# Kernel tuning notes

Measured on AMD Instinct MI355X. Metric: run time of the kernel, lower is better.

The kernel has to match this reference:

```python
import jax, jax.numpy as jnp
import numpy as np
from jax import lax

K = 3  # kernel_size


def _dynamic_conv(x, kernel, k, d):
    """Involution-style dynamic depthwise conv.
    x: [N,C,H,W], kernel: [N,C,k*k,H,W] per-pixel weights.
    Equivalent to (unfold(x, k, dilation=d, pad=k//2*d) * kernel).sum over tap dim,
    but computed as a fused shift-multiply-accumulate (no k^2-blowup intermediate).
    """
    H, W = x.shape[2], x.shape[3]
    pad = k // 2 * d
    xp = jnp.pad(x, ((0, 0), (0, 0), (pad, pad), (pad, pad)))
    acc = jnp.zeros_like(x)
    for idx in range(k * k):  # fixed small tap loop (9 taps)
        i, j = idx // k, idx % k
        patch = xp[:, :, i * d:i * d + H, j * d:j * d + W]  # [N,C,H,W]
        acc = acc + patch * kernel[:, :, idx]
    return acc


def setup_inputs() -> dict:
    key = jax.random.key(0)
    ks = jax.random.split(key, 6)
    N, C, H, W = 4, 64, 96, 96
    x = jax.random.normal(ks[0], (N, C, H, W), jnp.float32)
    y = jax.random.normal(ks[1], (N, C, H, W), jnp.float32)
    gen_w = jax.random.normal(ks[2], (3 * C * K * K, C), jnp.float32) * 0.05
    gen_b = jax.random.normal(ks[3], (3 * C * K * K,), jnp.float32) * 0.05
    fuse_w = jax.random.normal(ks[4], (C, 4 * C, 3, 3), jnp.float32) * 0.05
    fuse_b = jax.random.normal(ks[5], (C,), jnp.float32) * 0.05
    return {"x": x, "y": y, "gen_w": gen_w, "gen_b": gen_b,
            "fuse_w": fuse_w, "fuse_b": fuse_b}


def reference(x, y, gen_w, gen_b, fuse_w, fuse_b):
    N, C, H, W = x.shape
    # 1x1 conv kernel generator: [N, 3*C*K*K, H, W]
    kernels = jnp.einsum('nchw,oc->nohw', y, gen_w) + gen_b[None, :, None, None]
    kernels = kernels.reshape(N, 3, C, K * K, H, W)
    r1 = _dynamic_conv(x, kernels[:, 0], K, 1)
    r3 = _dynamic_conv(x, kernels[:, 1], K, 3)
    r5 = _dynamic_conv(x, kernels[:, 2], K, 5)
    cat = jnp.concatenate([x, r1, r3, r5], axis=1)  # [N,4C,H,W]
    out = lax.conv_general_dilated(
        cat, fuse_w, window_strides=(1, 1), padding=((1, 1), (1, 1)),
        dimension_numbers=('NCHW', 'OIHW', 'NCHW'))
    return out + fuse_b[None, :, None, None]
```

## Files before the change

kernel.cpp:

```cpp
#include <hip/hip_runtime.h>

typedef _Float16 f16;
typedef _Float16 f16x8 __attribute__((ext_vector_type(8)));
typedef _Float16 f16x4 __attribute__((ext_vector_type(4)));
typedef float f32x4 __attribute__((ext_vector_type(4)));

#define H 96
#define W 96
#define HWv (H * W)
#define PREC 9604
#define GWP_OFF  19668992
#define FWP_OFF  19890176

__device__ __forceinline__ size_t prec_rec(int n, int h, int w) {
    return (size_t)n * PREC + (size_t)(h + 1) * 98 + (w + 1);
}

__global__ __launch_bounds__(256) void prep_kernel(
    const float* __restrict__ gen_w, const float* __restrict__ fuse_w,
    unsigned char* __restrict__ ws)
{
    const int bid = blockIdx.x, tid = threadIdx.x;
    if (bid < 128) {
        const int gid = bid * 256 + tid;
        const int lane = gid & 63;
        if (gid < 18432) {
            const int rest = gid >> 6;
            const int s = rest & 7;
            const int rest2 = rest >> 3;
            const int tap = rest2 % 9, cot = rest2 / 9;
            const int co = cot * 16 + (lane & 15);
            const int ci0 = s * 32 + (lane >> 4) * 8;
            f16x8 v;
#pragma unroll
            for (int j = 0; j < 8; ++j)
                v[j] = (f16)fuse_w[(co * 256 + ci0 + j) * 9 + tap];
            reinterpret_cast<f16x8*>(ws + FWP_OFF)[rest * 64 + lane] = v;
        } else if (gid < 32256) {
            const int fid = gid - 18432;
            const int lane2 = fid & 63;
            const int rest = fid >> 6;
            const int T = rest >> 1, s = rest & 1;
            const int o = T * 16 + (lane2 & 15);
            const int cc0 = s * 32 + (lane2 >> 4) * 8;
            f16x8 v;
#pragma unroll
            for (int j = 0; j < 8; ++j)
                v[j] = (f16)gen_w[o * 64 + cc0 + j];
            reinterpret_cast<f16x8*>(ws + GWP_OFF)[rest * 64 + lane2] = v;
        }
    } else {
        const int idx0 = (bid - 128) * 256 + tid;
        for (int k = idx0; k < 49664; k += 32768) {
            const int rec = k >> 5, chunk = k & 31;
            const int n = rec / 388, rr = rec % 388;
            int r, c;
            if (rr < 196) { r = (rr < 98) ? 0 : 97; c = rr % 98; }
            else { const int k2 = rr - 196; c = (k2 < 96) ? 0 : 97; r = 1 + (k2 % 96); }
            const int4 z{0, 0, 0, 0};
            *reinterpret_cast<int4*>(
                ws + ((size_t)n * PREC + (size_t)r * 98 + c) * 512 + chunk * 16) = z;
        }
    }
}

__global__ __launch_bounds__(256, 5) void gen_dyn_kernel(
    const float* __restrict__ x, const float* __restrict__ y,
    const float* __restrict__ gen_b, unsigned char* __restrict__ ws)
{
    __shared__ __align__(16) unsigned char smem[25088];
    const int tid = threadIdx.x, lane = tid & 63, wv = tid >> 6;
    const int q4 = lane >> 4, px = lane & 15;
    const int bid = blockIdx.x;
    const int n = bid / 576, rem = bid % 576;
    const int h0 = rem / 6, w0 = (rem % 6) * 16;

    unsigned char* yls = smem;
    unsigned char* xls = smem + 2048;

    {
        const int scc = tid >> 2, sp4 = (tid & 3) * 4;
        const size_t gb = (size_t)(n * 64 + scc) * HWv + h0 * W + w0 + sp4;
        const f32x4 xv4 = *reinterpret_cast<const f32x4*>(x + gb);
        const f32x4 yv4 = *reinterpret_cast<const f32x4*>(y + gb);
#pragma unroll
        for (int k = 0; k < 4; ++k) {
            const int p = sp4 + k;
            const int off = (p * 128 + scc * 2) ^ ((p & 7) << 4);
            *reinterpret_cast<f16*>(xls + off) = (f16)xv4[k];
            *reinterpret_cast<f16*>(yls + off) = (f16)yv4[k];
        }
    }
    __syncthreads();
    if (tid < 128) {
        const int pxf = tid >> 3, c16 = tid & 7;
        const int4 v = *reinterpret_cast<const int4*>(
            xls + ((pxf * 128 + c16 * 16) ^ ((pxf & 7) << 4)));
        *reinterpret_cast<int4*>(ws + prec_rec(n, h0, w0 + pxf) * 512 + c16 * 16) = v;
    }
    f16x8 Bf[2];
#pragma unroll
    for (int s = 0; s < 2; ++s)
        Bf[s] = *reinterpret_cast<const f16x8*>(
            yls + ((px * 128 + s * 64 + q4 * 16) ^ ((px & 7) << 4)));
    __syncthreads();

    f16* klds = reinterpret_cast<f16*>(smem + 2048 + wv * 5760);
    f16* cs   = reinterpret_cast<f16*>(smem + wv * 512);
    const f16x8* gwp = reinterpret_cast<const f16x8*>(ws + GWP_OFF);
    const bool interior = (h0 >= 5) && (h0 <= 90) && (w0 >= 16) && (w0 <= 64);
    const int chl = lane >> 2, wu = lane & 3;

    for (int qi = 0; qi < 3; ++qi) {
        const int q = wv * 3 + qi;
#pragma unroll 3
        for (int t = 0; t < 9; ++t) {
            const int T = q * 9 + t;
            const f16x8 A0 = gwp[(T * 2 + 0) * 64 + lane];
            const f16x8 A1 = gwp[(T * 2 + 1) * 64 + lane];
            const f32x4 gb4 = *reinterpret_cast<const f32x4*>(gen_b + T * 16 + q4 * 4);
            f32x4 a = {0.f, 0.f, 0.f, 0.f};
            a = __builtin_amdgcn_mfma_f32_16x16x32_f16(A0, Bf[0], a, 0, 0, 0);
            a = __builtin_amdgcn_mfma_f32_16x16x32_f16(A1, Bf[1], a, 0, 0, 0);
#pragma unroll
            for (int r = 0; r < 4; ++r)
                klds[(t * 16 + q4 * 4 + r) * 20 + px] = (f16)(a[r] + gb4[r]);
        }
        asm volatile("s_waitcnt lgkmcnt(0)" ::: "memory");
        __builtin_amdgcn_sched_barrier(0);
        {
            const int ch = q * 16 + chl;
            const int bb = ch >> 6, c = ch & 63, d = 2 * bb + 1;
            const int wbase = w0 + wu * 4;
            const float* xc = x + (size_t)(n * 64 + c) * HWv;
            f32x4 racc = {0.f, 0.f, 0.f, 0.f};
            if (interior) {
#pragma unroll
                for (int tap = 0; tap < 9; ++tap) {
                    const f16x4 k4 = *reinterpret_cast<const f16x4*>(
                        &klds[(chl * 9 + tap) * 20 + wu * 4]);
                    const int hh = h0 + (tap / 3 - 1) * d;
                    const float* xr = xc + hh * W + wbase + (tap % 3 - 1) * d;
                    racc[0] = fmaf((float)k4[0], xr[0], racc[0]);
                    racc[1] = fmaf((float)k4[1], xr[1], racc[1]);
                    racc[2] = fmaf((float)k4[2], xr[2], racc[2]);
                    racc[3] = fmaf((float)k4[3], xr[3], racc[3]);
                }
            } else {
#pragma unroll
                for (int tap = 0; tap < 9; ++tap) {
                    const f16x4 k4 = *reinterpret_cast<const f16x4*>(
                        &klds[(chl * 9 + tap) * 20 + wu * 4]);
                    const int hh = h0 + (tap / 3 - 1) * d;
                    if (hh >= 0 && hh < H) {
                        const int wwb = wbase + (tap % 3 - 1) * d;
#pragma unroll
                        for (int kk = 0; kk < 4; ++kk) {
                            const int wk = wwb + kk;
                            if (wk >= 0 && wk < W)
                                racc[kk] = fmaf((float)k4[kk], xc[hh * W + wk], racc[kk]);
                        }
                    }
                }
            }
#pragma unroll
            for (int kk = 0; kk < 4; ++kk)
                cs[(wu * 4 + kk) * 16 + chl] = (f16)racc[kk];
        }
        asm volatile("s_waitcnt lgkmcnt(0)" ::: "memory");
        __builtin_amdgcn_sched_barrier(0);
        if (lane < 32) {
            const int pxf = lane >> 1, half = lane & 1;
            const int4 v = *reinterpret_cast<const int4*>(cs + pxf * 16 + half * 8);
            *reinterpret_cast<int4*>(
                ws + prec_rec(n, h0, w0 + pxf) * 512 + 128 + q * 32 + half * 16) = v;
        }
        __builtin_amdgcn_sched_barrier(0);
    }
}

__global__ __launch_bounds__(256, 3) void fuse_mfma_kernel(
    const unsigned char* __restrict__ ws, const float* __restrict__ fb,
    float* __restrict__ out)
{
    __shared__ __align__(16) unsigned char smem[13824];
    const int tid = threadIdx.x, lane = tid & 63, wv = tid >> 6;
    const int q4 = lane >> 4;
    const int bid = blockIdx.x;
    const int n = bid / 144, tile = bid % 144;
    const int h0 = (tile / 6) * 4, w0 = (tile % 6) * 16;
    const int pbp = wv & 1, coh = wv >> 1;

    const int e0 = tid, e1 = tid + 256;
    const int hpx0 = e0 >> 2, cc0 = e0 & 3;
    const int hpx1 = e1 >> 2, cc1 = e1 & 3;
    const size_t rb0 = prec_rec(n, h0 - 1 + hpx0 / 18, w0 - 1 + hpx0 % 18) * 512;
    const size_t rb1 = prec_rec(n, h0 - 1 + hpx1 / 18, w0 - 1 + hpx1 % 18) * 512;
    const int dso0 = hpx0 * 64 + ((cc0 * 16) ^ (((hpx0 >> 1) & 3) << 4));
    const int dso1 = hpx1 * 64 + ((cc1 * 16) ^ (((hpx1 >> 1) & 3) << 4));

    *reinterpret_cast<int4*>(smem + dso0) =
        *reinterpret_cast<const int4*>(ws + rb0 + cc0 * 16);
    if (tid < 176)
        *reinterpret_cast<int4*>(smem + dso1) =
            *reinterpret_cast<const int4*>(ws + rb1 + cc1 * 16);
    __syncthreads();

    f32x4 acc[2][2];
#pragma unroll
    for (int i = 0; i < 2; ++i)
#pragma unroll
        for (int j = 0; j < 2; ++j) acc[i][j] = {0.f, 0.f, 0.f, 0.f};

    const f16x8* fwp = reinterpret_cast<const f16x8*>(ws + FWP_OFF);

    for (int s = 0; s < 8; ++s) {
        unsigned char* buf  = smem + (s & 1) * 6912;
        unsigned char* nbuf = smem + ((s & 1) ^ 1) * 6912;
        int4 pf0{0,0,0,0}, pf1{0,0,0,0};
        if (s < 7) {
            pf0 = *reinterpret_cast<const int4*>(ws + rb0 + (s + 1) * 64 + cc0 * 16);
            if (tid < 176)
                pf1 = *reinterpret_cast<const int4*>(ws + rb1 + (s + 1) * 64 + cc1 * 16);
        }
        f16x8 B[4][3];
#pragma unroll
        for (int r = 0; r < 4; ++r)
#pragma unroll
            for (int cd = 0; cd < 3; ++cd) {
                const int hpx = (pbp * 2 + r) * 18 + (lane & 15) + cd;
                B[r][cd] = *reinterpret_cast<const f16x8*>(
                    buf + hpx * 64 + ((q4 * 16) ^ (((hpx >> 1) & 3) << 4)));
            }
#pragma unroll
        for (int tap = 0; tap < 9; ++tap) {
            const int rb = tap / 3, cd = tap % 3;
            f16x8 Af[2];
#pragma unroll
            for (int j = 0; j < 2; ++j)
                Af[j] = fwp[(((coh * 2 + j) * 9 + tap) * 8 + s) * 64 + lane];
#pragma unroll
            for (int i = 0; i < 2; ++i)
#pragma unroll
                for (int j = 0; j < 2; ++j)
                    acc[i][j] = __builtin_amdgcn_mfma_f32_16x16x32_f16(
                        Af[j], B[i + rb][cd], acc[i][j], 0, 0, 0);
        }
        if (s < 7) {
            *reinterpret_cast<int4*>(nbuf + dso0) = pf0;
            if (tid < 176)
                *reinterpret_cast<int4*>(nbuf + dso1) = pf1;
        }
        __syncthreads();
    }

#pragma unroll
    for (int i = 0; i < 2; ++i) {
        const int hh = h0 + pbp * 2 + i, ww = w0 + (lane & 15);
#pragma unroll
        for (int j = 0; j < 2; ++j) {
            const int co0 = (coh * 2 + j) * 16 + q4 * 4;
            const f32x4 fb4 = *reinterpret_cast<const f32x4*>(fb + co0);
#pragma unroll
            for (int r = 0; r < 4; ++r)
                out[(size_t)(n * 64 + co0 + r) * HWv + hh * W + ww]
                    = acc[i][j][r] + fb4[r];
        }
    }
}

extern "C" void kernel_launch(void* const* d_in, const int* in_sizes, int n_in,
                              void* d_out, int out_size, void* d_ws, size_t ws_size,
                              hipStream_t stream) {
    const float* x      = (const float*)d_in[0];
    const float* y      = (const float*)d_in[1];
    const float* gen_w  = (const float*)d_in[2];
    const float* gen_b  = (const float*)d_in[3];
    const float* fuse_w = (const float*)d_in[4];
    const float* fuse_b = (const float*)d_in[5];
    unsigned char* ws = (unsigned char*)d_ws;

    prep_kernel<<<256, 256, 0, stream>>>(gen_w, fuse_w, ws);
    gen_dyn_kernel<<<2304, 256, 0, stream>>>(x, y, gen_b, ws);
    fuse_mfma_kernel<<<576, 256, 0, stream>>>(ws, fuse_b, (float*)d_out);
}
```

Measured before the change: 202.5 us.

## Fuse kernel generation, dynamic conv and fuse conv into one tiled kernel

Result: slower. 495.9 us (+144.8%).

```diff
diff --git a/kernel.cpp b/kernel.cpp
--- a/kernel.cpp
+++ b/kernel.cpp
@@ -2,23 +2,18 @@
 
 typedef _Float16 f16;
 typedef _Float16 f16x8 __attribute__((ext_vector_type(8)));
-typedef _Float16 f16x4 __attribute__((ext_vector_type(4)));
 typedef float f32x4 __attribute__((ext_vector_type(4)));
 
 #define H 96
 #define W 96
 #define HWv (H * W)
 #define PREC 9604
-#define GWP_OFF  19668992
-#define FWP_OFF  19890176
-
-__device__ __forceinline__ size_t prec_rec(int n, int h, int w) {
-    return (size_t)n * PREC + (size_t)(h + 1) * 98 + (w + 1);
-}
+#define GWP_OFF 4917248
+#define FWP_OFF 5138432
 
 __global__ __launch_bounds__(256) void prep_kernel(
     const float* __restrict__ gen_w, const float* __restrict__ fuse_w,
-    unsigned char* __restrict__ ws)
+    const float* __restrict__ x, unsigned char* __restrict__ ws)
 {
     const int bid = blockIdx.x, tid = threadIdx.x;
     if (bid < 128) {
@@ -49,223 +44,202 @@
                 v[j] = (f16)gen_w[o * 64 + cc0 + j];
             reinterpret_cast<f16x8*>(ws + GWP_OFF)[rest * 64 + lane2] = v;
         }
+    } else if (bid < 2432) {
+        __shared__ __align__(16) unsigned char xls[2048];
+        const int tb = bid - 128;
+        const int n = tb / 576, rem = tb % 576;
+        const int h0 = rem / 6, w0 = (rem % 6) * 16;
+        const int scc = tid >> 2, sp4 = (tid & 3) * 4;
+        const f32x4 xv4 = *reinterpret_cast<const f32x4*>(
+            x + (size_t)(n * 64 + scc) * HWv + h0 * W + w0 + sp4);
+#pragma unroll
+        for (int k = 0; k < 4; ++k) {
+            const int p = sp4 + k;
+            *reinterpret_cast<f16*>(xls + ((p * 128 + scc * 2) ^ ((p & 7) << 4)))
+                = (f16)xv4[k];
+        }
+        __syncthreads();
+        if (tid < 128) {
+            const int pxf = tid >> 3, c16 = tid & 7;
+            const int4 v = *reinterpret_cast<const int4*>(
+                xls + ((pxf * 128 + c16 * 16) ^ ((pxf & 7) << 4)));
+            const size_t rec = (size_t)n * PREC + (size_t)(h0 + 1) * 98 + (w0 + pxf + 1);
+            *reinterpret_cast<int4*>(ws + rec * 128 + c16 * 16) = v;
+        }
     } else {
-        const int idx0 = (bid - 128) * 256 + tid;
-        for (int k = idx0; k < 49664; k += 32768) {
-            const int rec = k >> 5, chunk = k & 31;
+        const int idx = (bid - 2432) * 256 + tid;
+        if (idx < 12416) {
+            const int rec = idx >> 3, chunk = idx & 7;
             const int n = rec / 388, rr = rec % 388;
             int r, c;
             if (rr < 196) { r = (rr < 98) ? 0 : 97; c = rr % 98; }
             else { const int k2 = rr - 196; c = (k2 < 96) ? 0 : 97; r = 1 + (k2 % 96); }
             const int4 z{0, 0, 0, 0};
             *reinterpret_cast<int4*>(
-                ws + ((size_t)n * PREC + (size_t)r * 98 + c) * 512 + chunk * 16) = z;
+                ws + ((size_t)n * PREC + (size_t)r * 98 + c) * 128 + chunk * 16) = z;
         }
     }
 }
 
-__global__ __launch_bounds__(256, 5) void gen_dyn_kernel(
+__global__ __launch_bounds__(256, 2) void mega_kernel(
     const float* __restrict__ x, const float* __restrict__ y,
-    const float* __restrict__ gen_b, unsigned char* __restrict__ ws)
+    const float* __restrict__ gen_b, const unsigned char* __restrict__ ws,
+    const float* __restrict__ fb, float* __restrict__ out)
 {
-    __shared__ __align__(16) unsigned char smem[25088];
-    const int tid = threadIdx.x, lane = tid & 63, wv = tid >> 6;
-    const int q4 = lane >> 4, px = lane & 15;
-    const int bid = blockIdx.x;
-    const int n = bid / 576, rem = bid % 576;
-    const int h0 = rem / 6, w0 = (rem % 6) * 16;
-
-    unsigned char* yls = smem;
-    unsigned char* xls = smem + 2048;
-
-    {
-        const int scc = tid >> 2, sp4 = (tid & 3) * 4;
-        const size_t gb = (size_t)(n * 64 + scc) * HWv + h0 * W + w0 + sp4;
-        const f32x4 xv4 = *reinterpret_cast<const f32x4*>(x + gb);
-        const f32x4 yv4 = *reinterpret_cast<const f32x4*>(y + gb);
-#pragma unroll
-        for (int k = 0; k < 4; ++k) {
-            const int p = sp4 + k;
-            const int off = (p * 128 + scc * 2) ^ ((p & 7) << 4);
-            *reinterpret_cast<f16*>(xls + off) = (f16)xv4[k];
-            *reinterpret_cast<f16*>(yls + off) = (f16)yv4[k];
-        }
-    }
-    __syncthreads();
-    if (tid < 128) {
-        const int pxf = tid >> 3, c16 = tid & 7;
-        const int4 v = *reinterpret_cast<const int4*>(
-            xls + ((pxf * 128 + c16 * 16) ^ ((pxf & 7) << 4)));
-        *reinterpret_cast<int4*>(ws + prec_rec(n, h0, w0 + pxf) * 512 + c16 * 16) = v;
-    }
-    f16x8 Bf[2];
-#pragma unroll
-    for (int s = 0; s < 2; ++s)
-        Bf[s] = *reinterpret_cast<const f16x8*>(
-            yls + ((px * 128 + s * 64 + q4 * 16) ^ ((px & 7) << 4)));
-    __syncthreads();
-
-    f16* klds = reinterpret_cast<f16*>(smem + 2048 + wv * 5760);
-    f16* cs   = reinterpret_cast<f16*>(smem + wv * 512);
-    const f16x8* gwp = reinterpret_cast<const f16x8*>(ws + GWP_OFF);
-    const bool interior = (h0 >= 5) && (h0 <= 90) && (w0 >= 16) && (w0 <= 64);
-    const int chl = lane >> 2, wu = lane & 3;
-
-    for (int qi = 0; qi < 3; ++qi) {
-        const int q = wv * 3 + qi;
-#pragma unroll 3
-        for (int t = 0; t < 9; ++t) {
-            const int T = q * 9 + t;
-            const f16x8 A0 = gwp[(T * 2 + 0) * 64 + lane];
-            const f16x8 A1 = gwp[(T * 2 + 1) * 64 + lane];
-            const f32x4 gb4 = *reinterpret_cast<const f32x4*>(gen_b + T * 16 + q4 * 4);
-            f32x4 a = {0.f, 0.f, 0.f, 0.f};
-            a = __builtin_amdgcn_mfma_f32_16x16x32_f16(A0, Bf[0], a, 0, 0, 0);
-            a = __builtin_amdgcn_mfma_f32_16x16x32_f16(A1, Bf[1], a, 0, 0, 0);
-#pragma unroll
-            for (int r = 0; r < 4; ++r)
-                klds[(t * 16 + q4 * 4 + r) * 20 + px] = (f16)(a[r] + gb4[r]);
-        }
-        asm volatile("s_waitcnt lgkmcnt(0)" ::: "memory");
-        __builtin_amdgcn_sched_barrier(0);
-        {
-            const int ch = q * 16 + chl;
-            const int bb = ch >> 6, c = ch & 63, d = 2 * bb + 1;
-            const int wbase = w0 + wu * 4;
-            const float* xc = x + (size_t)(n * 64 + c) * HWv;
-            f32x4 racc = {0.f, 0.f, 0.f, 0.f};
-            if (interior) {
-#pragma unroll
-                for (int tap = 0; tap < 9; ++tap) {
-                    const f16x4 k4 = *reinterpret_cast<const f16x4*>(
-                        &klds[(chl * 9 + tap) * 20 + wu * 4]);
-                    const int hh = h0 + (tap / 3 - 1) * d;
-                    const float* xr = xc + hh * W + wbase + (tap % 3 - 1) * d;
-                    racc[0] = fmaf((float)k4[0], xr[0], racc[0]);
-                    racc[1] = fmaf((float)k4[1], xr[1], racc[1]);
-                    racc[2] = fmaf((float)k4[2], xr[2], racc[2]);
-                    racc[3] = fmaf((float)k4[3], xr[3], racc[3]);
-                }
-            } else {
-#pragma unroll
-                for (int tap = 0; tap < 9; ++tap) {
-                    const f16x4 k4 = *reinterpret_cast<const f16x4*>(
-                        &klds[(chl * 9 + tap) * 20 + wu * 4]);
-                    const int hh = h0 + (tap / 3 - 1) * d;
-                    if (hh >= 0 && hh < H) {
-                        const int wwb = wbase + (tap % 3 - 1) * d;
-#pragma unroll
-                        for (int kk = 0; kk < 4; ++kk) {
-                            const int wk = wwb + kk;
-                            if (wk >= 0 && wk < W)
-                                racc[kk] = fmaf((float)k4[kk], xc[hh * W + wk], racc[kk]);
-                        }
-                    }
-                }
-            }
-#pragma unroll
-            for (int kk = 0; kk < 4; ++kk)
-                cs[(wu * 4 + kk) * 16 + chl] = (f16)racc[kk];
-        }
-        asm volatile("s_waitcnt lgkmcnt(0)" ::: "memory");
-        __builtin_amdgcn_sched_barrier(0);
-        if (lane < 32) {
-            const int pxf = lane >> 1, half = lane & 1;
-            const int4 v = *reinterpret_cast<const int4*>(cs + pxf * 16 + half * 8);
-            *reinterpret_cast<int4*>(
-                ws + prec_rec(n, h0, w0 + pxf) * 512 + 128 + q * 32 + half * 16) = v;
-        }
-        __builtin_amdgcn_sched_barrier(0);
-    }
-}
-
-__global__ __launch_bounds__(256, 3) void fuse_mfma_kernel(
-    const unsigned char* __restrict__ ws, const float* __restrict__ fb,
-    float* __restrict__ out)
-{
-    __shared__ __align__(16) unsigned char smem[13824];
+    __shared__ __align__(16) unsigned char smem[78336];
     const int tid = threadIdx.x, lane = tid & 63, wv = tid >> 6;
     const int q4 = lane >> 4;
     const int bid = blockIdx.x;
     const int n = bid / 144, tile = bid % 144;
     const int h0 = (tile / 6) * 4, w0 = (tile % 6) * 16;
-    const int pbp = wv & 1, coh = wv >> 1;
-
-    const int e0 = tid, e1 = tid + 256;
-    const int hpx0 = e0 >> 2, cc0 = e0 & 3;
-    const int hpx1 = e1 >> 2, cc1 = e1 & 3;
-    const size_t rb0 = prec_rec(n, h0 - 1 + hpx0 / 18, w0 - 1 + hpx0 % 18) * 512;
-    const size_t rb1 = prec_rec(n, h0 - 1 + hpx1 / 18, w0 - 1 + hpx1 % 18) * 512;
-    const int dso0 = hpx0 * 64 + ((cc0 * 16) ^ (((hpx0 >> 1) & 3) << 4));
-    const int dso1 = hpx1 * 64 + ((cc1 * 16) ^ (((hpx1 >> 1) & 3) << 4));
-
-    *reinterpret_cast<int4*>(smem + dso0) =
-        *reinterpret_cast<const int4*>(ws + rb0 + cc0 * 16);
-    if (tid < 176)
-        *reinterpret_cast<int4*>(smem + dso1) =
-            *reinterpret_cast<const int4*>(ws + rb1 + cc1 * 16);
+    unsigned char* dyncat = smem + 36864;
+
+#pragma unroll
+    for (int it = 0; it < 27; ++it) {
+        const int e = tid + it * 256;
+        const int c = e / 108, px = e - c * 108;
+        const int r = px / 18, cc = px - r * 18;
+        int hh = h0 - 1 + r, ww = w0 - 1 + cc;
+        hh = hh < 0 ? 0 : (hh > 95 ? 95 : hh);
+        ww = ww < 0 ? 0 : (ww > 95 ? 95 : ww);
+        const float v = y[(size_t)(n * 64 + c) * HWv + hh * W + ww];
+        *reinterpret_cast<f16*>(smem + ((px * 128 + c * 2) ^ ((px & 7) << 4))) = (f16)v;
+    }
+    if (tid < 32) {
+        const int px = 108 + (tid >> 3), chunk = tid & 7;
+        const int4 z{0, 0, 0, 0};
+        *reinterpret_cast<int4*>(smem + ((px * 128 + chunk * 16) ^ ((px & 7) << 4))) = z;
+    }
     __syncthreads();
 
-    f32x4 acc[2][2];
-#pragma unroll
-    for (int i = 0; i < 2; ++i)
-#pragma unroll
-        for (int j = 0; j < 2; ++j) acc[i][j] = {0.f, 0.f, 0.f, 0.f};
+    f16x8 Bf[7][2];
+#pragma unroll
+    for (int nb = 0; nb < 7; ++nb)
+#pragma unroll
+        for (int s = 0; s < 2; ++s) {
+            const int px = nb * 16 + (lane & 15);
+            Bf[nb][s] = *reinterpret_cast<const f16x8*>(
+                smem + ((px * 128 + s * 64 + q4 * 16) ^ ((px & 7) << 4)));
+        }
+    __syncthreads();
+
+    const f16x8* gwp = reinterpret_cast<const f16x8*>(ws + GWP_OFF);
+
+    for (int g = 0; g < 12; ++g) {
+        {
+            const int ustart = wv * 16;
+            const int uend = (ustart + 16 < 63) ? ustart + 16 : 63;
+            int u = ustart;
+            while (u < uend) {
+                const int t = u / 7;
+                const int T = g * 9 + t;
+                const f16x8 A0 = gwp[(T * 2 + 0) * 64 + lane];
+                const f16x8 A1 = gwp[(T * 2 + 1) * 64 + lane];
+                const f32x4 gb4 = *reinterpret_cast<const f32x4*>(gen_b + T * 16 + q4 * 4);
+                const int nbe = (uend - t * 7 < 7) ? uend - t * 7 : 7;
+                for (int nb = u - t * 7; nb < nbe; ++nb, ++u) {
+                    f32x4 a = {0.f, 0.f, 0.f, 0.f};
+                    a = __builtin_amdgcn_mfma_f32_16x16x32_f16(A0, Bf[nb][0], a, 0, 0, 0);
+                    a = __builtin_amdgcn_mfma_f32_16x16x32_f16(A1, Bf[nb][1], a, 0, 0, 0);
+                    const int px = nb * 16 + (lane & 15);
+#pragma unroll
+                    for (int r = 0; r < 4; ++r) {
+                        const int o = t * 16 + q4 * 4 + r;
+                        *reinterpret_cast<f16*>(
+                            smem + ((o * 256 + px * 2) ^ ((o & 7) << 4)))
+                            = (f16)(a[r] + gb4[r]);
+                    }
+                }
+            }
+        }
+        __syncthreads();
+        {
+            const int chl = tid >> 4, pxt = tid & 15;
+            const int ch = g * 16 + chl;
+            const int bbr = ch >> 6, c = ch & 63, d = 2 * bbr + 1;
+            const float* xc = x + (size_t)(n * 64 + c) * HWv;
+#pragma unroll
+            for (int k = 0; k < 7; ++k) {
+                const int px = pxt + k * 16;
+                if (px < 108) {
+                    const int r = px / 18, cc = px - r * 18;
+                    const int hh = h0 - 1 + r, ww = w0 - 1 + cc;
+                    f16 res = (f16)0.f;
+                    if (hh >= 0 && hh < H && ww >= 0 && ww < W) {
+                        float acc = 0.f;
+#pragma unroll
+                        for (int tap = 0; tap < 9; ++tap) {
+                            const int o = chl * 9 + tap;
+                            const float kv = (float)*reinterpret_cast<const f16*>(
+                                smem + ((o * 256 + px * 2) ^ ((o & 7) << 4)));
+                            const int h2 = hh + (tap / 3 - 1) * d;
+                            const int w2 = ww + (tap % 3 - 1) * d;
+                            if (h2 >= 0 && h2 < H && w2 >= 0 && w2 < W)
+                                acc = fmaf(kv, xc[h2 * W + w2], acc);
+                        }
+                        res = (f16)acc;
+                    }
+                    *reinterpret_cast<f16*>(
+                        dyncat + ((px * 384 + ch * 2) ^ ((px & 7) << 4))) = res;
+                }
+            }
+        }
+        __syncthreads();
+    }
+
+#pragma unroll
+    for (int it = 0; it < 4; ++it) {
+        const int e = tid + it * 256;
+        if (e < 864) {
+            const int hpx = e >> 3, chunk = e & 7;
+            const int r = hpx / 18, cc = hpx - r * 18;
+            const size_t rec = (size_t)n * PREC + (size_t)(h0 + r) * 98 + (w0 + cc);
+            const int4 v = *reinterpret_cast<const int4*>(ws + rec * 128 + chunk * 16);
+            *reinterpret_cast<int4*>(
+                smem + ((hpx * 128 + chunk * 16) ^ ((hpx & 7) << 4))) = v;
+        }
+    }
+    __syncthreads();
+
+    f32x4 acc[4];
+#pragma unroll
+    for (int i = 0; i < 4; ++i) acc[i] = {0.f, 0.f, 0.f, 0.f};
 
     const f16x8* fwp = reinterpret_cast<const f16x8*>(ws + FWP_OFF);
-
     for (int s = 0; s < 8; ++s) {
-        unsigned char* buf  = smem + (s & 1) * 6912;
-        unsigned char* nbuf = smem + ((s & 1) ^ 1) * 6912;
-        int4 pf0{0,0,0,0}, pf1{0,0,0,0};
-        if (s < 7) {
-            pf0 = *reinterpret_cast<const int4*>(ws + rb0 + (s + 1) * 64 + cc0 * 16);
-            if (tid < 176)
-                pf1 = *reinterpret_cast<const int4*>(ws + rb1 + (s + 1) * 64 + cc1 * 16);
-        }
-        f16x8 B[4][3];
+        f16x8 B[6][3];
+#pragma unroll
+        for (int r = 0; r < 6; ++r)
+#pragma unroll
+            for (int dc = 0; dc < 3; ++dc) {
+                const int px = r * 18 + dc + (lane & 15);
+                if (s < 2) {
+                    B[r][dc] = *reinterpret_cast<const f16x8*>(
+                        smem + ((px * 128 + s * 64 + q4 * 16) ^ ((px & 7) << 4)));
+                } else {
+                    B[r][dc] = *reinterpret_cast<const f16x8*>(
+                        dyncat + ((px * 384 + (s - 2) * 64 + q4 * 16) ^ ((px & 7) << 4)));
+                }
+            }
+#pragma unroll
+        for (int tap = 0; tap < 9; ++tap) {
+            const int dr = tap / 3, dc = tap % 3;
+            const f16x8 Af = fwp[((wv * 9 + tap) * 8 + s) * 64 + lane];
+#pragma unroll
+            for (int nb = 0; nb < 4; ++nb)
+                acc[nb] = __builtin_amdgcn_mfma_f32_16x16x32_f16(
+                    Af, B[nb + dr][dc], acc[nb], 0, 0, 0);
+        }
+    }
+
+    const int co0 = wv * 16 + q4 * 4;
+    const f32x4 fb4 = *reinterpret_cast<const f32x4*>(fb + co0);
+#pragma unroll
+    for (int nb = 0; nb < 4; ++nb) {
+        const int hh = h0 + nb, ww = w0 + (lane & 15);
 #pragma unroll
         for (int r = 0; r < 4; ++r)
-#pragma unroll
-            for (int cd = 0; cd < 3; ++cd) {
-                const int hpx = (pbp * 2 + r) * 18 + (lane & 15) + cd;
-                B[r][cd] = *reinterpret_cast<const f16x8*>(
-                    buf + hpx * 64 + ((q4 * 16) ^ (((hpx >> 1) & 3) << 4)));
-            }
-#pragma unroll
-        for (int tap = 0; tap < 9; ++tap) {
-            const int rb = tap / 3, cd = tap % 3;
-            f16x8 Af[2];
-#pragma unroll
-            for (int j = 0; j < 2; ++j)
-                Af[j] = fwp[(((coh * 2 + j) * 9 + tap) * 8 + s) * 64 + lane];
-#pragma unroll
-            for (int i = 0; i < 2; ++i)
-#pragma unroll
-                for (int j = 0; j < 2; ++j)
-                    acc[i][j] = __builtin_amdgcn_mfma_f32_16x16x32_f16(
-                        Af[j], B[i + rb][cd], acc[i][j], 0, 0, 0);
-        }
-        if (s < 7) {
-            *reinterpret_cast<int4*>(nbuf + dso0) = pf0;
-            if (tid < 176)
-                *reinterpret_cast<int4*>(nbuf + dso1) = pf1;
-        }
-        __syncthreads();
-    }
-
-#pragma unroll
-    for (int i = 0; i < 2; ++i) {
-        const int hh = h0 + pbp * 2 + i, ww = w0 + (lane & 15);
-#pragma unroll
-        for (int j = 0; j < 2; ++j) {
-            const int co0 = (coh * 2 + j) * 16 + q4 * 4;
-            const f32x4 fb4 = *reinterpret_cast<const f32x4*>(fb + co0);
-#pragma unroll
-            for (int r = 0; r < 4; ++r)
-                out[(size_t)(n * 64 + co0 + r) * HWv + hh * W + ww]
-                    = acc[i][j][r] + fb4[r];
-        }
+            out[(size_t)(n * 64 + co0 + r) * HWv + hh * W + ww] = acc[nb][r] + fb4[r];
     }
 }
 
@@ -280,7 +254,6 @@
     const float* fuse_b = (const float*)d_in[5];
     unsigned char* ws = (unsigned char*)d_ws;
 
-    prep_kernel<<<256, 256, 0, stream>>>(gen_w, fuse_w, ws);
-    gen_dyn_kernel<<<2304, 256, 0, stream>>>(x, y, gen_b, ws);
-    fuse_mfma_kernel<<<576, 256, 0, stream>>>(ws, fuse_b, (float*)d_out);
+    prep_kernel<<<2481, 256, 0, stream>>>(gen_w, fuse_w, x, ws);
+    mega_kernel<<<576, 256, 0, stream>>>(x, y, gen_b, ws, fuse_b, (float*)d_out);
 }
```

## Stage x halo rows in LDS as fp16 for dynamic conv, remap blocks per XCD

Applied to the files above, without the earlier changes.

Measured after the change: 177.0 us. 1.14x faster.

```diff
diff --git a/kernel.cpp b/kernel.cpp
--- a/kernel.cpp
+++ b/kernel.cpp
@@ -64,39 +64,59 @@
     }
 }
 
-__global__ __launch_bounds__(256, 5) void gen_dyn_kernel(
+__global__ __launch_bounds__(256, 3) void gen_dyn_kernel(
     const float* __restrict__ x, const float* __restrict__ y,
     const float* __restrict__ gen_b, unsigned char* __restrict__ ws)
 {
-    __shared__ __align__(16) unsigned char smem[25088];
+    __shared__ __align__(16) unsigned char smem[50176];
     const int tid = threadIdx.x, lane = tid & 63, wv = tid >> 6;
     const int q4 = lane >> 4, px = lane & 15;
-    const int bid = blockIdx.x;
+    const int bid0 = blockIdx.x;
+    const int bid = (bid0 & 7) * 288 + (bid0 >> 3);
     const int n = bid / 576, rem = bid % 576;
     const int h0 = rem / 6, w0 = (rem % 6) * 16;
 
     unsigned char* yls = smem;
-    unsigned char* xls = smem + 2048;
+    f16* cs    = reinterpret_cast<f16*>(smem);
+    f16* klds  = reinterpret_cast<f16*>(smem + 2048 + wv * 5760);
+    f16* xhalo = reinterpret_cast<f16*>(smem + 25088);
 
     {
         const int scc = tid >> 2, sp4 = (tid & 3) * 4;
-        const size_t gb = (size_t)(n * 64 + scc) * HWv + h0 * W + w0 + sp4;
-        const f32x4 xv4 = *reinterpret_cast<const f32x4*>(x + gb);
-        const f32x4 yv4 = *reinterpret_cast<const f32x4*>(y + gb);
+        const f32x4 yv4 = *reinterpret_cast<const f32x4*>(
+            y + (size_t)(n * 64 + scc) * HWv + h0 * W + w0 + sp4);
 #pragma unroll
         for (int k = 0; k < 4; ++k) {
             const int p = sp4 + k;
-            const int off = (p * 128 + scc * 2) ^ ((p & 7) << 4);
-            *reinterpret_cast<f16*>(xls + off) = (f16)xv4[k];
-            *reinterpret_cast<f16*>(yls + off) = (f16)yv4[k];
+            *reinterpret_cast<f16*>(yls + ((p * 128 + scc * 2) ^ ((p & 7) << 4)))
+                = (f16)yv4[k];
+        }
+    }
+    for (int it = 0; it < 25; ++it) {
+        const int e = tid + it * 256;
+        if (e < 6272) {
+            const int j = e / 896;
+            const int r2 = e - j * 896;
+            const int ch = r2 / 14, p = r2 - ch * 14;
+            const int offj = (j < 3) ? 2 * j - 5 : ((j > 3) ? 2 * j - 7 : 0);
+            int hh = h0 + offj; hh = hh < 0 ? 0 : (hh > 95 ? 95 : hh);
+            int wb = w0 - 6 + p * 2; wb = wb < 0 ? 0 : (wb > 94 ? 94 : wb);
+            const float2 v = *reinterpret_cast<const float2*>(
+                x + (size_t)(n * 64 + ch) * HWv + hh * W + wb);
+            union { f16 h[2]; unsigned int u; } pk;
+            pk.h[0] = (f16)v.x; pk.h[1] = (f16)v.y;
+            *reinterpret_cast<unsigned int*>(&xhalo[(j * 64 + ch) * 28 + p * 2]) = pk.u;
         }
     }
     __syncthreads();
+
     if (tid < 128) {
-        const int pxf = tid >> 3, c16 = tid & 7;
-        const int4 v = *reinterpret_cast<const int4*>(
-            xls + ((pxf * 128 + c16 * 16) ^ ((pxf & 7) << 4)));
-        *reinterpret_cast<int4*>(ws + prec_rec(n, h0, w0 + pxf) * 512 + c16 * 16) = v;
+        const int pxr = tid >> 3, c8 = tid & 7;
+        union { f16 h[8]; int4 v; } pk;
+#pragma unroll
+        for (int jj = 0; jj < 8; ++jj)
+            pk.h[jj] = xhalo[(3 * 64 + c8 * 8 + jj) * 28 + pxr + 6];
+        *reinterpret_cast<int4*>(ws + prec_rec(n, h0, w0 + pxr) * 512 + c8 * 16) = pk.v;
     }
     f16x8 Bf[2];
 #pragma unroll
@@ -105,14 +125,12 @@
             yls + ((px * 128 + s * 64 + q4 * 16) ^ ((px & 7) << 4)));
     __syncthreads();
 
-    f16* klds = reinterpret_cast<f16*>(smem + 2048 + wv * 5760);
-    f16* cs   = reinterpret_cast<f16*>(smem + wv * 512);
     const f16x8* gwp = reinterpret_cast<const f16x8*>(ws + GWP_OFF);
     const bool interior = (h0 >= 5) && (h0 <= 90) && (w0 >= 16) && (w0 <= 64);
     const int chl = lane >> 2, wu = lane & 3;
 
     for (int qi = 0; qi < 3; ++qi) {
-        const int q = wv * 3 + qi;
+        const int q = qi * 4 + wv;
 #pragma unroll 3
         for (int t = 0; t < 9; ++t) {
             const int T = q * 9 + t;
@@ -131,51 +149,52 @@
         {
             const int ch = q * 16 + chl;
             const int bb = ch >> 6, c = ch & 63, d = 2 * bb + 1;
-            const int wbase = w0 + wu * 4;
-            const float* xc = x + (size_t)(n * 64 + c) * HWv;
             f32x4 racc = {0.f, 0.f, 0.f, 0.f};
             if (interior) {
 #pragma unroll
                 for (int tap = 0; tap < 9; ++tap) {
                     const f16x4 k4 = *reinterpret_cast<const f16x4*>(
                         &klds[(chl * 9 + tap) * 20 + wu * 4]);
-                    const int hh = h0 + (tap / 3 - 1) * d;
-                    const float* xr = xc + hh * W + wbase + (tap % 3 - 1) * d;
-                    racc[0] = fmaf((float)k4[0], xr[0], racc[0]);
-                    racc[1] = fmaf((float)k4[1], xr[1], racc[1]);
-                    racc[2] = fmaf((float)k4[2], xr[2], racc[2]);
-                    racc[3] = fmaf((float)k4[3], xr[3], racc[3]);
+                    const int ti = tap / 3 - 1, tj = tap % 3 - 1;
+                    const int j = 3 + ti * (bb + 1);
+                    const f16* xr = &xhalo[(j * 64 + c) * 28 + wu * 4 + tj * d + 6];
+                    racc[0] = fmaf((float)k4[0], (float)xr[0], racc[0]);
+                    racc[1] = fmaf((float)k4[1], (float)xr[1], racc[1]);
+                    racc[2] = fmaf((float)k4[2], (float)xr[2], racc[2]);
+                    racc[3] = fmaf((float)k4[3], (float)xr[3], racc[3]);
                 }
             } else {
 #pragma unroll
                 for (int tap = 0; tap < 9; ++tap) {
                     const f16x4 k4 = *reinterpret_cast<const f16x4*>(
                         &klds[(chl * 9 + tap) * 20 + wu * 4]);
-                    const int hh = h0 + (tap / 3 - 1) * d;
+                    const int ti = tap / 3 - 1, tj = tap % 3 - 1;
+                    const int j = 3 + ti * (bb + 1);
+                    const int hh = h0 + ti * d;
                     if (hh >= 0 && hh < H) {
-                        const int wwb = wbase + (tap % 3 - 1) * d;
+                        const f16* xr = &xhalo[(j * 64 + c) * 28 + wu * 4 + tj * d + 6];
+                        const int wwb = w0 + wu * 4 + tj * d;
 #pragma unroll
                         for (int kk = 0; kk < 4; ++kk) {
                             const int wk = wwb + kk;
                             if (wk >= 0 && wk < W)
-                                racc[kk] = fmaf((float)k4[kk], xc[hh * W + wk], racc[kk]);
+                                racc[kk] = fmaf((float)k4[kk], (float)xr[kk], racc[kk]);
                         }
                     }
                 }
             }
 #pragma unroll
             for (int kk = 0; kk < 4; ++kk)
-                cs[(wu * 4 + kk) * 16 + chl] = (f16)racc[kk];
-        }
-        asm volatile("s_waitcnt lgkmcnt(0)" ::: "memory");
-        __builtin_amdgcn_sched_barrier(0);
-        if (lane < 32) {
-            const int pxf = lane >> 1, half = lane & 1;
-            const int4 v = *reinterpret_cast<const int4*>(cs + pxf * 16 + half * 8);
+                cs[(wu * 4 + kk) * 64 + wv * 16 + chl] = (f16)racc[kk];
+        }
+        __syncthreads();
+        if (tid < 128) {
+            const int pxr = tid >> 3, c8 = tid & 7;
+            const int4 v = *reinterpret_cast<const int4*>(&cs[pxr * 64 + c8 * 8]);
             *reinterpret_cast<int4*>(
-                ws + prec_rec(n, h0, w0 + pxf) * 512 + 128 + q * 32 + half * 16) = v;
-        }
-        __builtin_amdgcn_sched_barrier(0);
+                ws + prec_rec(n, h0, w0 + pxr) * 512 + 128 + qi * 128 + c8 * 16) = v;
+        }
+        __syncthreads();
     }
 }
 
@@ -186,7 +205,8 @@
     __shared__ __align__(16) unsigned char smem[13824];
     const int tid = threadIdx.x, lane = tid & 63, wv = tid >> 6;
     const int q4 = lane >> 4;
-    const int bid = blockIdx.x;
+    const int bid0 = blockIdx.x;
+    const int bid = (bid0 & 7) * 72 + (bid0 >> 3);
     const int n = bid / 144, tile = bid % 144;
     const int h0 = (tile / 6) * 4, w0 = (tile % 6) * 16;
     const int pbp = wv & 1, coh = wv >> 1;
```
